# Performance work log

Measured on AMD Instinct MI355X. Metric: run time of the kernel, lower is better.

## Reference

```python
import jax, jax.numpy as jnp
import numpy as np

N, M, NNZ, D = 50000, 20000, 400000, 256
ALPHA, BETA = 0.1, 0.5


def setup_inputs() -> dict:
    key = jax.random.key(0)
    ks = jax.random.split(key, 7)
    X = jax.random.normal(ks[0], (N, D), dtype=jnp.float32)
    X0 = jax.random.normal(ks[1], (N, D), dtype=jnp.float32)
    W = jax.random.normal(ks[2], (D, D), dtype=jnp.float32) / np.sqrt(D)
    degV = jax.random.uniform(ks[3], (N, 1), dtype=jnp.float32, minval=0.1, maxval=1.0)
    degE = jax.random.uniform(ks[4], (M, 1), dtype=jnp.float32, minval=0.1, maxval=1.0)
    vertex = jax.random.randint(ks[5], (NNZ,), 0, N, dtype=jnp.int32)
    edges = jax.random.randint(ks[6], (NNZ,), 0, M, dtype=jnp.int32)
    alpha = jnp.float32(ALPHA)
    beta = jnp.float32(BETA)
    return {"X": X, "X0": X0, "W": W, "degV": degV, "degE": degE,
            "vertex": vertex, "edges": edges, "alpha": alpha, "beta": beta}


def _normalize_l2(X):
    # torch: rownorm is detached -> treat scale as constant w.r.t. grad
    rownorm = jax.lax.stop_gradient(jnp.linalg.norm(X, axis=1, keepdims=True))
    scale = jnp.where(rownorm > 0, 1.0 / rownorm, 0.0)
    return X * scale


def reference(X, X0, W, degV, degE, vertex, edges, alpha, beta):
    # hop 1: gather node features to incidences, mean-aggregate into hyperedges
    Xve = X[vertex]                                               # [NNZ, D]
    sums = jax.ops.segment_sum(Xve, edges, num_segments=M)        # [M, D]
    cnts = jax.ops.segment_sum(jnp.ones((NNZ,), X.dtype), edges, num_segments=M)
    Xe = sums / jnp.maximum(cnts, 1.0)[:, None]                   # mean (first_aggregate)
    Xe = Xe * degE
    # hop 2: gather edge features back to incidences, sum-aggregate into nodes
    Xev = Xe[edges]                                               # [NNZ, D]
    Xv = jax.ops.segment_sum(Xev, vertex, num_segments=N)         # [N, D]
    Xv = Xv * degV
    Xn = _normalize_l2(Xv)                                        # use_norm=True
    Xi = (1.0 - alpha) * Xn + alpha * X0
    out = (1.0 - beta) * Xi + beta * (Xi @ W)
    return out
```

## Files before the change

### kernel.cpp

```cpp
#include <hip/hip_runtime.h>
#include <cstdint>

static constexpr int DD = 256;
static constexpr int SNB = 64;

typedef unsigned short ushort_t;
typedef __attribute__((ext_vector_type(8))) short short8v;
typedef __attribute__((ext_vector_type(4))) float f32x4;

static __device__ inline ushort_t f2bf(float f) {
  uint32_t u = __builtin_bit_cast(uint32_t, f);
  uint32_t r = (u + 0x7fffu + ((u >> 16) & 1u)) >> 16;
  return (ushort_t)r;
}
static __device__ inline float bf2f(ushort_t u) {
  return __builtin_bit_cast(float, (uint32_t)u << 16);
}
static __device__ inline void addbf8(float* a, int4 x) {
  uint32_t ux = (uint32_t)x.x, uy = (uint32_t)x.y;
  uint32_t uz = (uint32_t)x.z, uw = (uint32_t)x.w;
  a[0] += __builtin_bit_cast(float, ux << 16);
  a[1] += __builtin_bit_cast(float, ux & 0xFFFF0000u);
  a[2] += __builtin_bit_cast(float, uy << 16);
  a[3] += __builtin_bit_cast(float, uy & 0xFFFF0000u);
  a[4] += __builtin_bit_cast(float, uz << 16);
  a[5] += __builtin_bit_cast(float, uz & 0xFFFF0000u);
  a[6] += __builtin_bit_cast(float, uw << 16);
  a[7] += __builtin_bit_cast(float, uw & 0xFFFF0000u);
}


__global__ __launch_bounds__(256) void k_prep(const float* __restrict__ W,
                                              ushort_t* __restrict__ Wt,
                                              ushort_t* __restrict__ XeZ,
                                              ushort_t* __restrict__ XbfZ,
                                              const float* __restrict__ X,
                                              ushort_t* __restrict__ Xbf, int total4,
                                              const int* __restrict__ vertex,
                                              const int* __restrict__ edges,
                                              int* __restrict__ cntV,
                                              int* __restrict__ cntE, int nnz,
                                              int xb) {
  int b = blockIdx.x;
  if (b < 256) {
    int t = b * 256 + threadIdx.x;
    int k = t >> 8, c = t & 255;
    Wt[c * 256 + k] = f2bf(W[t]);
    if (b == 0) {
      int4 z = make_int4(0, 0, 0, 0);
      if (threadIdx.x < 32)       reinterpret_cast<int4*>(XeZ)[threadIdx.x] = z;
      else if (threadIdx.x < 64)  reinterpret_cast<int4*>(XbfZ)[threadIdx.x - 32] = z;
    }
  } else if (b < 256 + xb) {
    int i = (b - 256) * 256 + threadIdx.x;
    if (i < total4) {
      float4 v = reinterpret_cast<const float4*>(X)[i];
      ushort4 r;
      r.x = f2bf(v.x); r.y = f2bf(v.y); r.z = f2bf(v.z); r.w = f2bf(v.w);
      reinterpret_cast<ushort4*>(Xbf)[i] = r;
    }
  } else {
    int i = (b - 256 - xb) * 256 + threadIdx.x;
    if (i < nnz) {
      atomicAdd(&cntV[vertex[i]], 1);
      atomicAdd(&cntE[edges[i]], 1);
    }
  }
}

__device__ inline int wave_incl_scan(int v, int lane) {
  #pragma unroll
  for (int o = 1; o < 64; o <<= 1) {
    int u = __shfl_up(v, o);
    if (lane >= o) v += u;
  }
  return v;
}

__global__ __launch_bounds__(256) void k_bsum(const int* __restrict__ cntE,
                                              const int* __restrict__ cntV,
                                              int* __restrict__ bsum, int M, int N) {
  int arr = blockIdx.x >> 6;
  int b = blockIdx.x & 63;
  const int* cnt = arr ? cntV : cntE;
  int n = arr ? N : M;
  int chunk = (((n + SNB - 1) / SNB) + 3) & ~3;
  int lo = b * chunk, hi = min(lo + chunk, n);
  int s = 0;
  for (int i = lo + (int)threadIdx.x; i < hi; i += 256) s += cnt[i];
  #pragma unroll
  for (int o = 32; o; o >>= 1) s += __shfl_down(s, o);
  __shared__ int sh[4];
  if ((threadIdx.x & 63) == 0) sh[threadIdx.x >> 6] = s;
  __syncthreads();
  if (threadIdx.x == 0) bsum[blockIdx.x] = sh[0] + sh[1] + sh[2] + sh[3];
}

__global__ __launch_bounds__(128) void k_bscan(const int* __restrict__ bsum,
                                               int* __restrict__ bpre,
                                               int* __restrict__ offsE, int* __restrict__ offsV,
                                               int M, int N) {
  int t = threadIdx.x;
  int lane = t & 63;
  int v = bsum[t];
  int inc = wave_incl_scan(v, lane);
  bpre[t] = inc - v;
  if (lane == 63) {
    if (t < 64) offsE[M] = inc;
    else        offsV[N] = inc;
  }
}

__global__ __launch_bounds__(256) void k_woffs(const int* __restrict__ cntE,
                                               const int* __restrict__ cntV,
                                               const int* __restrict__ bpre,
                                               int* __restrict__ offsE, int* __restrict__ curE,
                                               int* __restrict__ offsV, int* __restrict__ curV,
                                               int M, int N) {
  int arr = blockIdx.x >> 6;
  int b = blockIdx.x & 63;
  const int* cnt = arr ? cntV : cntE;
  int* offs = arr ? offsV : offsE;
  int* cur  = arr ? curV  : curE;
  int n = arr ? N : M;
  int chunk = (((n + SNB - 1) / SNB) + 3) & ~3;
  int lo = b * chunk, hi = min(lo + chunk, n);
  if (lo >= n) return;
  int base = bpre[blockIdx.x];

  int idx = lo + (int)threadIdx.x * 4;
  int c0 = 0, c1 = 0, c2 = 0, c3 = 0;
  if (idx + 3 < hi) {
    int4 c = *reinterpret_cast<const int4*>(cnt + idx);
    c0 = c.x; c1 = c.y; c2 = c.z; c3 = c.w;
  } else if (idx < hi) {
    c0 = cnt[idx];
    if (idx + 1 < hi) c1 = cnt[idx + 1];
    if (idx + 2 < hi) c2 = cnt[idx + 2];
  }
  int tsum = c0 + c1 + c2 + c3;
  int lane = threadIdx.x & 63, wid = threadIdx.x >> 6;
  int winc = wave_incl_scan(tsum, lane);
  __shared__ int wtot[4];
  if (lane == 63) wtot[wid] = winc;
  __syncthreads();
  int wbase = 0;
  #pragma unroll
  for (int q = 0; q < 4; ++q) wbase += (q < wid) ? wtot[q] : 0;
  int excl = base + wbase + winc - tsum;
  int o0 = excl, o1 = o0 + c0, o2 = o1 + c1, o3 = o2 + c2;
  if (idx + 3 < hi) {
    *reinterpret_cast<int4*>(offs + idx) = make_int4(o0, o1, o2, o3);
    *reinterpret_cast<int4*>(cur + idx)  = make_int4(o0, o1, o2, o3);
  } else if (idx < hi) {
    offs[idx] = o0; cur[idx] = o0;
    if (idx + 1 < hi) { offs[idx + 1] = o1; cur[idx + 1] = o1; }
    if (idx + 2 < hi) { offs[idx + 2] = o2; cur[idx + 2] = o2; }
  }
}


__global__ void k_fill(const int* __restrict__ vertex, const int* __restrict__ edges,
                       int* __restrict__ curE, int* __restrict__ curV,
                       ushort_t* __restrict__ incEv, ushort_t* __restrict__ incVe, int nnz) {
  int i = blockIdx.x * blockDim.x + threadIdx.x;
  if (i < nnz) {
    int v = vertex[i], e = edges[i];
    int pe = atomicAdd(&curE[e], 1);
    incEv[pe] = (ushort_t)v;
    int pv = atomicAdd(&curV[v], 1);
    incVe[pv] = (ushort_t)e;
  }
}


__global__ void k_hop1(const ushort_t* __restrict__ Xbf, const float* __restrict__ degE,
                       const int* __restrict__ offsE, const ushort_t* __restrict__ incEv,
                       ushort_t* __restrict__ Xe, int M) {
  int gw = (blockIdx.x * blockDim.x + threadIdx.x) >> 6;
  int lane = threadIdx.x & 63;
  if (gw >= M) return;
  int half = lane >> 5, sub = lane & 31;
  int s = offsE[gw], t = offsE[gw + 1];
  float acc[8] = {0.f, 0.f, 0.f, 0.f, 0.f, 0.f, 0.f, 0.f};
  const ushort_t* rowbase = Xbf + sub * 8;
  int k = s;
  for (; k + 8 <= t; k += 8) {
    int4 x[4];
    #pragma unroll
    for (int p = 0; p < 4; ++p) {
      int lo = incEv[k + 2 * p], hi = incEv[k + 2 * p + 1];
      int v = half ? hi : lo;
      x[p] = *reinterpret_cast<const int4*>(rowbase + (size_t)v * DD);
    }
    #pragma unroll
    for (int p = 0; p < 4; ++p) addbf8(acc, x[p]);
  }
  for (; k < t; k += 2) {
    int idx = k + half;
    if (idx < t) {
      int v = incEv[idx];
      int4 x = *reinterpret_cast<const int4*>(rowbase + (size_t)v * DD);
      addbf8(acc, x);
    }
  }
  #pragma unroll
  for (int j = 0; j < 8; ++j) acc[j] += __shfl_xor(acc[j], 32);
  float scale = degE[gw] / fmaxf((float)(t - s), 1.0f);
  float b0 = half ? acc[4] : acc[0];
  float b1 = half ? acc[5] : acc[1];
  float b2 = half ? acc[6] : acc[2];
  float b3 = half ? acc[7] : acc[3];
  ushort4 r;
  r.x = f2bf(b0 * scale); r.y = f2bf(b1 * scale);
  r.z = f2bf(b2 * scale); r.w = f2bf(b3 * scale);
  *reinterpret_cast<ushort4*>(Xe + (size_t)gw * DD + sub * 8 + half * 4) = r;
}


__global__ void k_hop2(const ushort_t* __restrict__ Xe, const float* __restrict__ X0,
                       const float* __restrict__ degV, const int* __restrict__ offsV,
                       const ushort_t* __restrict__ incVe, const float* __restrict__ alpha_p,
                       float* __restrict__ Xi, int N) {
  int gw = (blockIdx.x * blockDim.x + threadIdx.x) >> 6;
  int lane = threadIdx.x & 63;
  if (gw >= N) return;
  int half = lane >> 5, sub = lane & 31;
  int s = offsV[gw], t = offsV[gw + 1];
  float acc[8] = {0.f, 0.f, 0.f, 0.f, 0.f, 0.f, 0.f, 0.f};
  const ushort_t* rowbase = Xe + sub * 8;
  int k = s;
  for (; k + 8 <= t; k += 8) {
    int4 x[4];
    #pragma unroll
    for (int p = 0; p < 4; ++p) {
      int lo = incVe[k + 2 * p], hi = incVe[k + 2 * p + 1];
      int e = half ? hi : lo;
      x[p] = *reinterpret_cast<const int4*>(rowbase + (size_t)e * DD);
    }
    #pragma unroll
    for (int p = 0; p < 4; ++p) addbf8(acc, x[p]);
  }
  for (; k < t; k += 2) {
    int idx = k + half;
    if (idx < t) {
      int e = incVe[idx];
      int4 x = *reinterpret_cast<const int4*>(rowbase + (size_t)e * DD);
      addbf8(acc, x);
    }
  }
  #pragma unroll
  for (int j = 0; j < 8; ++j) acc[j] += __shfl_xor(acc[j], 32);
  float dv = degV[gw];
  float b0 = (half ? acc[4] : acc[0]) * dv;
  float b1 = (half ? acc[5] : acc[1]) * dv;
  float b2 = (half ? acc[6] : acc[2]) * dv;
  float b3 = (half ? acc[7] : acc[3]) * dv;
  float ss = b0 * b0 + b1 * b1 + b2 * b2 + b3 * b3;
  #pragma unroll
  for (int o = 1; o < 64; o <<= 1) ss += __shfl_xor(ss, o);
  float norm = sqrtf(ss);
  float scl = (norm > 0.f) ? (1.0f / norm) : 0.f;
  float a = alpha_p[0];
  float oma = 1.0f - a;
  int f0 = sub * 8 + half * 4;
  float4 x0 = *reinterpret_cast<const float4*>(X0 + (size_t)gw * DD + f0);
  float4 r;
  r.x = oma * (b0 * scl) + a * x0.x;
  r.y = oma * (b1 * scl) + a * x0.y;
  r.z = oma * (b2 * scl) + a * x0.z;
  r.w = oma * (b3 * scl) + a * x0.w;
  *reinterpret_cast<float4*>(Xi + (size_t)gw * DD + f0) = r;
}


__global__ __launch_bounds__(512, 4) void k_gemm_mfma(float* XiOut,
                                                      const ushort_t* __restrict__ Wt,
                                                      const float* __restrict__ beta_p,
                                                      int nrows) {
  __shared__ ushort_t A_lds[128][36];
  __shared__ ushort_t B_lds[256][36];
  const int tid = threadIdx.x;
  const int lane = tid & 63;
  const int wid = tid >> 6;
  const int wr = wid >> 2;
  const int wc = wid & 3;
  const int l15 = lane & 15;
  const int l4  = lane >> 4;
  const int row0 = blockIdx.x * 128;

  const int t2   = tid & 1;
  const int arow = tid >> 1;

  f32x4 acc[4][4];
  #pragma unroll
  for (int m = 0; m < 4; ++m)
    #pragma unroll
    for (int n = 0; n < 4; ++n) acc[m][n] = (f32x4){0.f, 0.f, 0.f, 0.f};

  for (int k0 = 0; k0 < 256; k0 += 32) {
    if (arow < 128) {
      int grow = row0 + arow;
      float4 v0 = make_float4(0.f, 0.f, 0.f, 0.f), v1 = v0, v2 = v0, v3 = v0;
      if (grow < nrows) {
        const float* src = XiOut + (size_t)grow * 256 + k0 + t2 * 16;
        v0 = *reinterpret_cast<const float4*>(src + 0);
        v1 = *reinterpret_cast<const float4*>(src + 4);
        v2 = *reinterpret_cast<const float4*>(src + 8);
        v3 = *reinterpret_cast<const float4*>(src + 12);
      }
      uint4 pk0, pk1;
      pk0.x = (uint32_t)f2bf(v0.x) | ((uint32_t)f2bf(v0.y) << 16);
      pk0.y = (uint32_t)f2bf(v0.z) | ((uint32_t)f2bf(v0.w) << 16);
      pk0.z = (uint32_t)f2bf(v1.x) | ((uint32_t)f2bf(v1.y) << 16);
      pk0.w = (uint32_t)f2bf(v1.z) | ((uint32_t)f2bf(v1.w) << 16);
      pk1.x = (uint32_t)f2bf(v2.x) | ((uint32_t)f2bf(v2.y) << 16);
      pk1.y = (uint32_t)f2bf(v2.z) | ((uint32_t)f2bf(v2.w) << 16);
      pk1.z = (uint32_t)f2bf(v3.x) | ((uint32_t)f2bf(v3.y) << 16);
      pk1.w = (uint32_t)f2bf(v3.z) | ((uint32_t)f2bf(v3.w) << 16);
      *reinterpret_cast<uint4*>(&A_lds[arow][t2 * 16 + 0]) = pk0;
      *reinterpret_cast<uint4*>(&A_lds[arow][t2 * 16 + 8]) = pk1;
    }
    {
      const ushort_t* src = Wt + (size_t)arow * 256 + k0 + t2 * 16;
      int4 w0 = *reinterpret_cast<const int4*>(src + 0);
      int4 w1 = *reinterpret_cast<const int4*>(src + 8);
      *reinterpret_cast<int4*>(&B_lds[arow][t2 * 16 + 0]) = w0;
      *reinterpret_cast<int4*>(&B_lds[arow][t2 * 16 + 8]) = w1;
    }
    __syncthreads();
    short8v a[4], b[4];
    #pragma unroll
    for (int m = 0; m < 4; ++m)
      a[m] = *reinterpret_cast<const short8v*>(&A_lds[wr * 64 + m * 16 + l15][l4 * 8]);
    #pragma unroll
    for (int n = 0; n < 4; ++n)
      b[n] = *reinterpret_cast<const short8v*>(&B_lds[wc * 64 + n * 16 + l15][l4 * 8]);
    #pragma unroll
    for (int m = 0; m < 4; ++m)
      #pragma unroll
      for (int n = 0; n < 4; ++n)
        acc[m][n] = __builtin_amdgcn_mfma_f32_16x16x32_bf16(a[m], b[n], acc[m][n], 0, 0, 0);
    __syncthreads();
  }

  float b = beta_p[0], ob = 1.0f - b;
  int rb0 = row0 + wr * 64;
  int cb0 = wc * 64;
  #pragma unroll
  for (int m = 0; m < 4; ++m) {
    #pragma unroll
    for (int j = 0; j < 4; ++j) {
      int r = rb0 + m * 16 + l4 * 4 + j;
      if (r < nrows) {
        #pragma unroll
        for (int n = 0; n < 4; ++n) {
          size_t idx = (size_t)r * 256 + cb0 + n * 16 + l15;
          float xi = XiOut[idx];
          XiOut[idx] = ob * xi + b * acc[m][n][j];
        }
      }
    }
  }
}


extern "C" void kernel_launch(void* const* d_in, const int* in_sizes, int n_in,
                              void* d_out, int out_size, void* d_ws, size_t ws_size,
                              hipStream_t stream) {
  const float* X     = (const float*)d_in[0];
  const float* X0    = (const float*)d_in[1];
  const float* W     = (const float*)d_in[2];
  const float* degV  = (const float*)d_in[3];
  const float* degE  = (const float*)d_in[4];
  const int*   vertex= (const int*)d_in[5];
  const int*   edges = (const int*)d_in[6];
  const float* alpha = (const float*)d_in[7];
  const float* beta  = (const float*)d_in[8];

  const int N   = in_sizes[3];
  const int M   = in_sizes[4];
  const int NNZ = in_sizes[5];

  auto r4 = [](int x) { return (x + 3) & ~3; };
  const int Mr = r4(M), Nr = r4(N);

  int* w = (int*)d_ws;
  int* cntE  = w; w += Mr;
  int* cntV  = w; w += Nr;
  int* offsE = w; w += r4(M + 1);
  int* offsV = w; w += r4(N + 1);
  int* curE  = w; w += Mr;
  int* curV  = w; w += Nr;
  int* bsum  = w; w += 128;
  int* bpre  = w; w += 128;
  ushort_t* incEv16 = (ushort_t*)w; w += (NNZ + 1) / 2;
  ushort_t* incVe16 = (ushort_t*)w; w += (NNZ + 1) / 2;
  uintptr_t p = (uintptr_t)w;
  p = (p + 15) & ~(uintptr_t)15;
  ushort_t* Wt = (ushort_t*)p;
  p += (size_t)256 * 256 * sizeof(ushort_t);
  ushort_t* Xe = (ushort_t*)p;

  float*    Xi  = (float*)d_out;
  ushort_t* Xbf = (ushort_t*)d_out;

  hipMemsetAsync(cntE, 0, (size_t)(Mr + Nr) * sizeof(int), stream);

  int nb = (NNZ + 255) / 256;
  int xb = (N * (DD / 4) + 255) / 256;
  k_prep<<<256 + xb + nb, 256, 0, stream>>>(W, Wt, Xe + (size_t)M * DD,
                                            Xbf + (size_t)N * DD, X, Xbf, N * (DD / 4),
                                            vertex, edges, cntV, cntE, NNZ, xb);
  k_bsum <<<2 * SNB, 256, 0, stream>>>(cntE, cntV, bsum, M, N);
  k_bscan<<<1, 128, 0, stream>>>(bsum, bpre, offsE, offsV, M, N);
  k_woffs<<<2 * SNB, 256, 0, stream>>>(cntE, cntV, bpre, offsE, curE, offsV, curV, M, N);
  k_fill <<<nb, 256, 0, stream>>>(vertex, edges, curE, curV, incEv16, incVe16, NNZ);

  k_hop1<<<(M + 3) / 4, 256, 0, stream>>>(Xbf, degE, offsE, incEv16, Xe, M);
  k_hop2<<<(N + 3) / 4, 256, 0, stream>>>(Xe, X0, degV, offsV, incVe16, alpha, Xi, N);
  k_gemm_mfma<<<(N + 127) / 128, 512, 0, stream>>>(Xi, Wt, beta, N);
}
```

Baseline: 200.9 us.

## Fold beta residual into W, merge scan kernels and fuse prep into fill

Folds the (1-beta)*Xi + beta*Xi@W epilogue into a modified weight matrix (beta*W + (1-beta)*I), so the GEMM epilogue no longer reads Xi back from global memory. Merges the block-prefix scan into the offset-writing kernel, with each block recomputing the 128-entry scan in shared memory. Moves the X-to-bf16 conversion and W transpose into the fill kernel and splits counting into its own kernel. This removes one launch and one full read of the output, but the identity term now passes through bf16 rounding, and the padding-row zeroing done by the old prep kernel is dropped.

```diff
diff --git a/kernel.cpp b/kernel.cpp
--- a/kernel.cpp
+++ b/kernel.cpp
@@ -30,41 +30,12 @@
 }
 
 
-__global__ __launch_bounds__(256) void k_prep(const float* __restrict__ W,
-                                              ushort_t* __restrict__ Wt,
-                                              ushort_t* __restrict__ XeZ,
-                                              ushort_t* __restrict__ XbfZ,
-                                              const float* __restrict__ X,
-                                              ushort_t* __restrict__ Xbf, int total4,
-                                              const int* __restrict__ vertex,
-                                              const int* __restrict__ edges,
-                                              int* __restrict__ cntV,
-                                              int* __restrict__ cntE, int nnz,
-                                              int xb) {
-  int b = blockIdx.x;
-  if (b < 256) {
-    int t = b * 256 + threadIdx.x;
-    int k = t >> 8, c = t & 255;
-    Wt[c * 256 + k] = f2bf(W[t]);
-    if (b == 0) {
-      int4 z = make_int4(0, 0, 0, 0);
-      if (threadIdx.x < 32)       reinterpret_cast<int4*>(XeZ)[threadIdx.x] = z;
-      else if (threadIdx.x < 64)  reinterpret_cast<int4*>(XbfZ)[threadIdx.x - 32] = z;
-    }
-  } else if (b < 256 + xb) {
-    int i = (b - 256) * 256 + threadIdx.x;
-    if (i < total4) {
-      float4 v = reinterpret_cast<const float4*>(X)[i];
-      ushort4 r;
-      r.x = f2bf(v.x); r.y = f2bf(v.y); r.z = f2bf(v.z); r.w = f2bf(v.w);
-      reinterpret_cast<ushort4*>(Xbf)[i] = r;
-    }
-  } else {
-    int i = (b - 256 - xb) * 256 + threadIdx.x;
-    if (i < nnz) {
-      atomicAdd(&cntV[vertex[i]], 1);
-      atomicAdd(&cntE[edges[i]], 1);
-    }
+__global__ void k_count(const int* __restrict__ vertex, const int* __restrict__ edges,
+                        int* __restrict__ cntV, int* __restrict__ cntE, int nnz) {
+  int i = blockIdx.x * blockDim.x + threadIdx.x;
+  if (i < nnz) {
+    atomicAdd(&cntV[vertex[i]], 1);
+    atomicAdd(&cntE[edges[i]], 1);
   }
 }
 
@@ -96,27 +67,25 @@
   if (threadIdx.x == 0) bsum[blockIdx.x] = sh[0] + sh[1] + sh[2] + sh[3];
 }
 
-__global__ __launch_bounds__(128) void k_bscan(const int* __restrict__ bsum,
-                                               int* __restrict__ bpre,
-                                               int* __restrict__ offsE, int* __restrict__ offsV,
-                                               int M, int N) {
-  int t = threadIdx.x;
-  int lane = t & 63;
-  int v = bsum[t];
-  int inc = wave_incl_scan(v, lane);
-  bpre[t] = inc - v;
-  if (lane == 63) {
-    if (t < 64) offsE[M] = inc;
-    else        offsV[N] = inc;
-  }
-}
-
-__global__ __launch_bounds__(256) void k_woffs(const int* __restrict__ cntE,
-                                               const int* __restrict__ cntV,
-                                               const int* __restrict__ bpre,
-                                               int* __restrict__ offsE, int* __restrict__ curE,
-                                               int* __restrict__ offsV, int* __restrict__ curV,
-                                               int M, int N) {
+__global__ __launch_bounds__(256) void k_woffs2(const int* __restrict__ cntE,
+                                                const int* __restrict__ cntV,
+                                                const int* __restrict__ bsum,
+                                                int* __restrict__ offsE, int* __restrict__ curE,
+                                                int* __restrict__ offsV, int* __restrict__ curV,
+                                                int M, int N) {
+  __shared__ int sbpre[128];
+  int tid = threadIdx.x;
+  if (tid < 128) {
+    int v = bsum[tid];
+    int inc = wave_incl_scan(v, tid & 63);
+    sbpre[tid] = inc - v;
+    if (blockIdx.x == 0 && (tid & 63) == 63) {
+      if (tid < 64) offsE[M] = inc;
+      else          offsV[N] = inc;
+    }
+  }
+  __syncthreads();
+
   int arr = blockIdx.x >> 6;
   int b = blockIdx.x & 63;
   const int* cnt = arr ? cntV : cntE;
@@ -126,7 +95,7 @@
   int chunk = (((n + SNB - 1) / SNB) + 3) & ~3;
   int lo = b * chunk, hi = min(lo + chunk, n);
   if (lo >= n) return;
-  int base = bpre[blockIdx.x];
+  int base = sbpre[blockIdx.x];
 
   int idx = lo + (int)threadIdx.x * 4;
   int c0 = 0, c1 = 0, c2 = 0, c3 = 0;
@@ -160,16 +129,38 @@
 }
 
 
-__global__ void k_fill(const int* __restrict__ vertex, const int* __restrict__ edges,
-                       int* __restrict__ curE, int* __restrict__ curV,
-                       ushort_t* __restrict__ incEv, ushort_t* __restrict__ incVe, int nnz) {
-  int i = blockIdx.x * blockDim.x + threadIdx.x;
-  if (i < nnz) {
-    int v = vertex[i], e = edges[i];
-    int pe = atomicAdd(&curE[e], 1);
-    incEv[pe] = (ushort_t)v;
-    int pv = atomicAdd(&curV[v], 1);
-    incVe[pv] = (ushort_t)e;
+__global__ void k_fillx(const int* __restrict__ vertex, const int* __restrict__ edges,
+                        int* __restrict__ curE, int* __restrict__ curV,
+                        ushort_t* __restrict__ incEv, ushort_t* __restrict__ incVe,
+                        int nnz, int nb,
+                        const float* __restrict__ X, ushort_t* __restrict__ Xbf,
+                        int total4, int xb,
+                        const float* __restrict__ W, const float* __restrict__ beta_p,
+                        ushort_t* __restrict__ Wt) {
+  int b = blockIdx.x;
+  if (b < nb) {
+    int i = b * 256 + (int)threadIdx.x;
+    if (i < nnz) {
+      int v = vertex[i], e = edges[i];
+      int pe = atomicAdd(&curE[e], 1);
+      incEv[pe] = (ushort_t)v;
+      int pv = atomicAdd(&curV[v], 1);
+      incVe[pv] = (ushort_t)e;
+    }
+  } else if (b < nb + xb) {
+    int i = (b - nb) * 256 + (int)threadIdx.x;
+    if (i < total4) {
+      float4 v = reinterpret_cast<const float4*>(X)[i];
+      ushort4 r;
+      r.x = f2bf(v.x); r.y = f2bf(v.y); r.z = f2bf(v.z); r.w = f2bf(v.w);
+      reinterpret_cast<ushort4*>(Xbf)[i] = r;
+    }
+  } else {
+    int t = (b - nb - xb) * 256 + (int)threadIdx.x;
+    int k = t >> 8, c = t & 255;
+    float beta = beta_p[0];
+    float val = beta * W[t] + ((k == c) ? (1.0f - beta) : 0.0f);
+    Wt[c * 256 + k] = f2bf(val);
   }
 }
 
@@ -276,7 +267,6 @@
 
 __global__ __launch_bounds__(512, 4) void k_gemm_mfma(float* XiOut,
                                                       const ushort_t* __restrict__ Wt,
-                                                      const float* __restrict__ beta_p,
                                                       int nrows) {
   __shared__ ushort_t A_lds[128][36];
   __shared__ ushort_t B_lds[256][36];
@@ -344,7 +334,6 @@
     __syncthreads();
   }
 
-  float b = beta_p[0], ob = 1.0f - b;
   int rb0 = row0 + wr * 64;
   int cb0 = wc * 64;
   #pragma unroll
@@ -356,8 +345,7 @@
         #pragma unroll
         for (int n = 0; n < 4; ++n) {
           size_t idx = (size_t)r * 256 + cb0 + n * 16 + l15;
-          float xi = XiOut[idx];
-          XiOut[idx] = ob * xi + b * acc[m][n][j];
+          XiOut[idx] = acc[m][n][j];
         }
       }
     }
@@ -393,7 +381,6 @@
   int* curE  = w; w += Mr;
   int* curV  = w; w += Nr;
   int* bsum  = w; w += 128;
-  int* bpre  = w; w += 128;
   ushort_t* incEv16 = (ushort_t*)w; w += (NNZ + 1) / 2;
   ushort_t* incVe16 = (ushort_t*)w; w += (NNZ + 1) / 2;
   uintptr_t p = (uintptr_t)w;
@@ -408,16 +395,17 @@
   hipMemsetAsync(cntE, 0, (size_t)(Mr + Nr) * sizeof(int), stream);
 
   int nb = (NNZ + 255) / 256;
-  int xb = (N * (DD / 4) + 255) / 256;
-  k_prep<<<256 + xb + nb, 256, 0, stream>>>(W, Wt, Xe + (size_t)M * DD,
-                                            Xbf + (size_t)N * DD, X, Xbf, N * (DD / 4),
-                                            vertex, edges, cntV, cntE, NNZ, xb);
-  k_bsum <<<2 * SNB, 256, 0, stream>>>(cntE, cntV, bsum, M, N);
-  k_bscan<<<1, 128, 0, stream>>>(bsum, bpre, offsE, offsV, M, N);
-  k_woffs<<<2 * SNB, 256, 0, stream>>>(cntE, cntV, bpre, offsE, curE, offsV, curV, M, N);
-  k_fill <<<nb, 256, 0, stream>>>(vertex, edges, curE, curV, incEv16, incVe16, NNZ);
+  int total4 = N * (DD / 4);
+  int xb = (total4 + 255) / 256;
+  k_count <<<nb, 256, 0, stream>>>(vertex, edges, cntV, cntE, NNZ);
+  k_bsum  <<<2 * SNB, 256, 0, stream>>>(cntE, cntV, bsum, M, N);
+  k_woffs2<<<2 * SNB, 256, 0, stream>>>(cntE, cntV, bsum, offsE, curE, offsV, curV, M, N);
+  k_fillx <<<nb + xb + 256, 256, 0, stream>>>(vertex, edges, curE, curV,
+                                              incEv16, incVe16, NNZ, nb,
+                                              X, Xbf, total4, xb,
+                                              W, beta, Wt);
 
   k_hop1<<<(M + 3) / 4, 256, 0, stream>>>(Xbf, degE, offsE, incEv16, Xe, M);
   k_hop2<<<(N + 3) / 4, 256, 0, stream>>>(Xe, X0, degV, offsV, incVe16, alpha, Xi, N);
-  k_gemm_mfma<<<(N + 127) / 128, 512, 0, stream>>>(Xi, Wt, beta, N);
-}
+  k_gemm_mfma<<<(N + 127) / 128, 512, 0, stream>>>(Xi, Wt, N);
+}
```

Measured after the change: 192.2 us (median of 2 runs). -4.4%, faster.
